# Kernel optimization log

Hardware: AMD Instinct MI355X
Metric: run time of the kernel (lower is better)

Reference implementation:

```python
import jax, jax.numpy as jnp
import numpy as np
from jax import lax

THR = 1.0
SLOPE = 25.0
EPS = 1e-5

@jax.custom_vjp
def spike(u):
    # Heaviside with fast-sigmoid surrogate gradient (slope=25)
    return (u > 0.0).astype(u.dtype)

def _spike_fwd(u):
    return (u > 0.0).astype(u.dtype), u

def _spike_bwd(u, g):
    return (g / (SLOPE * jnp.abs(u) + 1.0) ** 2,)

spike.defvjp(_spike_fwd, _spike_bwd)

def lif_scan(inp, beta):
    # inp: (T, B, H); snntorch Leaky, reset_mechanism='subtract', init mem=0
    def step(mem, cur):
        reset = lax.stop_gradient(spike(mem - THR))
        mem = beta * mem + cur - reset * THR
        spk = spike(mem - THR)
        return mem, (spk, mem)
    mem0 = jnp.zeros(inp.shape[1:], inp.dtype)
    _, (spk, mem) = lax.scan(step, mem0, inp)
    return spk, mem

def bn_per_step(h, g, b):
    # h: (T, B, H); training-mode BatchNorm1d applied per timestep over batch
    m = h.mean(axis=1, keepdims=True)
    v = h.var(axis=1, keepdims=True)
    return (h - m) / jnp.sqrt(v + EPS) * g + b

def setup_inputs() -> dict:
    key = jax.random.key(0)
    ks = jax.random.split(key, 16)
    B, T, C = 128, 128, 32
    H, Ts, HOR, K = 512, 4, 96, 3
    s = 0.02
    return {
        "x": jax.random.normal(ks[0], (B, T, C), jnp.float32),
        "conv_w": jax.random.normal(ks[1], (H * Ts, C, K), jnp.float32) * s,
        "conv_b": jnp.zeros((H * Ts,), jnp.float32),
        "bn1_g": jnp.ones((H * Ts,), jnp.float32),
        "bn1_b": jnp.zeros((H * Ts,), jnp.float32),
        "beta_enc": jnp.full((H,), 0.9, jnp.float32),
        "bn2_g": jnp.ones((H,), jnp.float32),
        "bn2_b": jnp.zeros((H,), jnp.float32),
        "beta2": jnp.full((H,), 0.9, jnp.float32),
        "bn3_g": jnp.ones((H,), jnp.float32),
        "bn3_b": jnp.zeros((H,), jnp.float32),
        "beta3": jnp.full((H,), 0.9, jnp.float32),
        "wq": jax.random.normal(ks[2], (H, H), jnp.float32) * s,
        "bq": jnp.zeros((H,), jnp.float32),
        "wk": jax.random.normal(ks[3], (H, H), jnp.float32) * s,
        "bk": jnp.zeros((H,), jnp.float32),
        "wv": jax.random.normal(ks[4], (H, H), jnp.float32) * s,
        "bv": jnp.zeros((H,), jnp.float32),
        "bna_g": jnp.ones((H,), jnp.float32),
        "bna_b": jnp.zeros((H,), jnp.float32),
        "wh": jax.random.normal(ks[5], (HOR, H), jnp.float32) * s,
        "bh": jnp.zeros((HOR,), jnp.float32),
    }

def reference(x, conv_w, conv_b, bn1_g, bn1_b, beta_enc, bn2_g, bn2_b, beta2,
              bn3_g, bn3_b, beta3, wq, bq, wk, bk, wv, bv, bna_g, bna_b, wh, bh):
    B, T, C = x.shape
    H = beta2.shape[0]
    Ts = conv_w.shape[0] // H
    # Conv spike encoder: Conv1d(C -> H*Ts, k, pad=k//2)
    k = conv_w.shape[2]
    h = lax.conv_general_dilated(x.transpose(0, 2, 1), conv_w, (1,), [(k // 2, k // 2)],
                                 dimension_numbers=("NCH", "OIH", "NCH"))
    h = h + conv_b[None, :, None]  # (B, H*Ts, T)
    # BatchNorm1d (training mode): stats over (B, T) per channel, biased var
    m = h.mean((0, 2), keepdims=True)
    v = h.var((0, 2), keepdims=True)
    h = (h - m) / jnp.sqrt(v + EPS) * bn1_g[None, :, None] + bn1_b[None, :, None]
    # (B, H*Ts, T) -> (T*Ts, B, H)
    h = h.transpose(0, 2, 1).reshape(B, T, Ts, H).reshape(B, T * Ts, H).transpose(1, 0, 2)
    spk_enc, _ = lif_scan(h, jnp.clip(beta_enc, 0.0, 0.99))
    # bn2 -> lif2 -> bn3 -> lif3 (BN applied per step in the torch loop)
    h2 = bn_per_step(spk_enc, bn2_g, bn2_b)
    s2, _ = lif_scan(h2, jnp.clip(beta2, 0.0, 0.99))
    h3 = bn_per_step(s2, bn3_g, bn3_b)
    _, mem3 = lif_scan(h3, jnp.clip(beta3, 0.0, 0.99))  # (Ttot, B, H)
    # Spiking attention over membrane trajectory
    xa = mem3.transpose(1, 0, 2)  # (B, Ttot, H)
    Q = xa @ wq.T + bq
    K = xa @ wk.T + bk
    V = xa @ wv.T + bv
    attn = jax.nn.sigmoid(jnp.einsum("btd,bsd->bts", Q, K) * (H ** -0.5))
    feat = jnp.einsum("bts,bsd->btd", attn, V).mean(axis=1)  # (B, H)
    mf = feat.mean(0, keepdims=True)
    vf = feat.var(0, keepdims=True)
    feat = (feat - mf) / jnp.sqrt(vf + EPS) * bna_g + bna_b
    return feat @ wh.T + bh  # (B, horizon)
```

## Files before the change

### kernel.cpp

```cpp
#include <hip/hip_runtime.h>
#include <math.h>

#define EPSF 1e-5f

static constexpr int Bn   = 128;
static constexpr int Tn   = 128;
static constexpr int Cn   = 32;
static constexpr int On   = 2048;
static constexpr int Hn   = 512;
static constexpr int TTn  = 512;
static constexpr int HORn = 96;
static constexpr int BH   = Bn * Hn;
static constexpr float THRf = 1.0f;

__device__ __forceinline__ float bf2f(unsigned short u) {
    union { unsigned int i; float f; } v; v.i = ((unsigned int)u) << 16; return v.f;
}
__device__ __forceinline__ unsigned short f2bf(float f) {
    union { float f; unsigned int i; } v; v.f = f;
    unsigned int r = v.i + 0x7fff + ((v.i >> 16) & 1);
    return (unsigned short)(r >> 16);
}

using bfrag  = __attribute__((ext_vector_type(8))) short;
using f32x4v = __attribute__((ext_vector_type(4))) float;
using f32x16 = __attribute__((ext_vector_type(16))) float;
using us8v   = __attribute__((ext_vector_type(8))) unsigned short;

#define GLD16(gp, lp) __builtin_amdgcn_global_load_lds( \
    (const __attribute__((address_space(1))) void*)(gp), \
    (__attribute__((address_space(3))) void*)(lp), 16, 0, 0)

__global__ __launch_bounds__(256) void im2col_k(const float* __restrict__ x,
    unsigned short* __restrict__ Ph, unsigned short* __restrict__ Pl)
{
    int idx = blockIdx.x * 256 + threadIdx.x;
    int row = idx / 96, kc = idx - row * 96;
    int k = kc >> 5, c = kc & 31;
    int t = row & 127, b = row >> 7;
    int tg = t + k - 1;
    float v = (tg >= 0 && tg < Tn) ? x[((size_t)b * Tn + tg) * Cn + c] : 0.f;
    unsigned short hi = f2bf(v);
    Ph[idx] = hi;
    Pl[idx] = f2bf(v - bf2f(hi));
}

__global__ __launch_bounds__(256) void wprep_k(const float* __restrict__ wconv,
    unsigned short* __restrict__ Wh, unsigned short* __restrict__ Wl)
{
    int idx = blockIdx.x * 256 + threadIdx.x;
    int o = idx / 96, kc = idx - o * 96;
    int k = kc >> 5, c = kc & 31;
    float v = wconv[(size_t)o * 96 + c * 3 + k];
    unsigned short hi = f2bf(v);
    Wh[idx] = hi;
    Wl[idx] = f2bf(v - bf2f(hi));
}

__global__ __launch_bounds__(256) void conv_mfma_k(
    const unsigned short* __restrict__ Ph, const unsigned short* __restrict__ Pl,
    const unsigned short* __restrict__ Wh, const unsigned short* __restrict__ Wl,
    float* __restrict__ raw, float* __restrict__ sums)
{
    const int b  = blockIdx.x;
    const int n0 = blockIdx.y * 128;
    const int tid = threadIdx.x;
    const int lane = tid & 63;
    const int quad = lane >> 4, lr = lane & 15;
    const int wid = tid >> 6, wm = wid & 1, wn = wid >> 1;

    f32x4v acc[4][4] = {};
#pragma unroll
    for (int ks = 0; ks < 3; ks++) {
        const int col = ks * 32 + quad * 8;
        bfrag ah[4], al[4], bh[4], bl[4];
#pragma unroll
        for (int mi = 0; mi < 4; mi++) {
            size_t roff = ((size_t)b * 128 + wm * 64 + mi * 16 + lr) * 96 + col;
            ah[mi] = *(const bfrag*)(Ph + roff);
            al[mi] = *(const bfrag*)(Pl + roff);
        }
#pragma unroll
        for (int ni = 0; ni < 4; ni++) {
            size_t roff = (size_t)(n0 + wn * 64 + ni * 16 + lr) * 96 + col;
            bh[ni] = *(const bfrag*)(Wh + roff);
            bl[ni] = *(const bfrag*)(Wl + roff);
        }
#pragma unroll
        for (int mi = 0; mi < 4; mi++)
#pragma unroll
            for (int ni = 0; ni < 4; ni++) {
                acc[mi][ni] = __builtin_amdgcn_mfma_f32_16x16x32_bf16(
                    ah[mi], bh[ni], acc[mi][ni], 0, 0, 0);
                acc[mi][ni] = __builtin_amdgcn_mfma_f32_16x16x32_bf16(
                    ah[mi], bl[ni], acc[mi][ni], 0, 0, 0);
                acc[mi][ni] = __builtin_amdgcn_mfma_f32_16x16x32_bf16(
                    al[mi], bh[ni], acc[mi][ni], 0, 0, 0);
            }
    }
#pragma unroll
    for (int ni = 0; ni < 4; ni++) {
        int o = n0 + wn * 64 + ni * 16 + lr;
        int ts = o >> 9, hh = o & 511;
        float s = 0.f, ss = 0.f;
#pragma unroll
        for (int mi = 0; mi < 4; mi++)
#pragma unroll
            for (int r = 0; r < 4; r++) {
                int t = wm * 64 + mi * 16 + quad * 4 + r;
                float v = acc[mi][ni][r];
                raw[((size_t)(t * 4 + ts) * Bn + b) * Hn + hh] = v;
                s += v; ss += v * v;
            }
        s  += __shfl_xor(s, 16);  s  += __shfl_xor(s, 32);
        ss += __shfl_xor(ss, 16); ss += __shfl_xor(ss, 32);
        if (quad == 0) {
            atomicAdd(&sums[o], s);
            atomicAdd(&sums[On + o], ss);
        }
    }
}

__global__ void bn1_final_k(const float* __restrict__ sums,
                            const float* __restrict__ g, const float* __restrict__ bb,
                            float* __restrict__ scale, float* __restrict__ shift)
{
    int o = blockIdx.x * 256 + threadIdx.x;
    float m = sums[o] * (1.f / 16384.f);
    float v = sums[On + o] * (1.f / 16384.f) - m * m;
    float sc = g[o] / sqrtf(v + EPSF);
    scale[o] = sc;
    shift[o] = bb[o] - m * sc;
}

__global__ __launch_bounds__(256) void lif1_k(const float* __restrict__ raw,
    const float* __restrict__ scale, const float* __restrict__ shift,
    const float* __restrict__ beta_in, unsigned char* __restrict__ spk)
{
    const int thr = blockIdx.x * 256 + threadIdx.x;
    const int hh = thr & 511;
    const float beta = fminf(fmaxf(beta_in[hh], 0.f), 0.99f);
    float sc[4], sh[4];
#pragma unroll
    for (int ts = 0; ts < 4; ts++) { sc[ts] = scale[ts * Hn + hh]; sh[ts] = shift[ts * Hn + hh]; }
    float mem = 0.f;
    for (int tt = 0; tt < TTn; tt += 8) {
        float cu[8];
#pragma unroll
        for (int u = 0; u < 8; u++) cu[u] = raw[(size_t)(tt + u) * BH + thr];
#pragma unroll
        for (int u = 0; u < 8; u++) {
            float cur = cu[u] * sc[u & 3] + sh[u & 3];
            float reset = mem > THRf ? 1.f : 0.f;
            mem = beta * mem + cur - reset;
            spk[(size_t)(tt + u) * BH + thr] = mem > THRf ? (unsigned char)1 : (unsigned char)0;
        }
    }
}

__global__ __launch_bounds__(256) void bnstep_k(const unsigned char* __restrict__ spk,
    const float* __restrict__ g, const float* __restrict__ bb,
    float* __restrict__ av, float* __restrict__ zv)
{
    const int tt = blockIdx.x;
    const int h0 = threadIdx.x * 2;
    int c0 = 0, c1 = 0;
    const unsigned char* base = spk + (size_t)tt * BH + h0;
#pragma unroll 8
    for (int b = 0; b < Bn; b++) {
        unsigned short v = *(const unsigned short*)(base + (size_t)b * Hn);
        c0 += (v & 0xff); c1 += (v >> 8);
    }
#pragma unroll
    for (int q = 0; q < 2; q++) {
        int hh = h0 + q;
        float p = (q ? c1 : c0) * (1.f / 128.f);
        float inv = 1.f / sqrtf(p - p * p + EPSF);
        float gi = g[hh] * inv;
        float zz = bb[hh] - p * gi;
        av[(size_t)tt * Hn + hh] = gi + zz;
        zv[(size_t)tt * Hn + hh] = zz;
    }
}

__global__ __launch_bounds__(256) void lif2_k(const unsigned char* __restrict__ sin_,
    const float* __restrict__ av, const float* __restrict__ zv,
    const float* __restrict__ beta_in, unsigned char* __restrict__ sout)
{
    const int thr = blockIdx.x * 256 + threadIdx.x;
    const int hh = thr & 511;
    const float beta = fminf(fmaxf(beta_in[hh], 0.f), 0.99f);
    float mem = 0.f;
    for (int tt = 0; tt < TTn; tt += 8) {
        float aa[8], zz[8]; unsigned char ss[8];
#pragma unroll
        for (int u = 0; u < 8; u++) {
            ss[u] = sin_[(size_t)(tt + u) * BH + thr];
            aa[u] = av[(size_t)(tt + u) * Hn + hh];
            zz[u] = zv[(size_t)(tt + u) * Hn + hh];
        }
#pragma unroll
        for (int u = 0; u < 8; u++) {
            float cur = ss[u] ? aa[u] : zz[u];
            float reset = mem > THRf ? 1.f : 0.f;
            mem = beta * mem + cur - reset;
            sout[(size_t)(tt + u) * BH + thr] = mem > THRf ? (unsigned char)1 : (unsigned char)0;
        }
    }
}

__global__ __launch_bounds__(256) void lif3_k(const unsigned char* __restrict__ sin_,
    const float* __restrict__ av, const float* __restrict__ zv,
    const float* __restrict__ beta_in, unsigned short* __restrict__ mem3b)
{
    const int thr = blockIdx.x * 256 + threadIdx.x;
    const int hh = thr & 511;
    const int b = thr >> 9;
    const float beta = fminf(fmaxf(beta_in[hh], 0.f), 0.99f);
    float mem = 0.f;
    for (int tt = 0; tt < TTn; tt += 8) {
        float aa[8], zz[8]; unsigned char ss[8];
#pragma unroll
        for (int u = 0; u < 8; u++) {
            ss[u] = sin_[(size_t)(tt + u) * BH + thr];
            aa[u] = av[(size_t)(tt + u) * Hn + hh];
            zz[u] = zv[(size_t)(tt + u) * Hn + hh];
        }
#pragma unroll
        for (int u = 0; u < 8; u++) {
            float cur = ss[u] ? aa[u] : zz[u];
            float reset = mem > THRf ? 1.f : 0.f;
            mem = beta * mem + cur - reset;
            mem3b[((size_t)b * TTn + (tt + u)) * Hn + hh] = f2bf(mem);
        }
    }
}

__global__ __launch_bounds__(256) void gemm_atb_k(const float* __restrict__ Aw,
    const float* __restrict__ Bw, float* __restrict__ GTp)
{
    __shared__ float As[8][132];
    __shared__ float Bs[8][132];
    const int m0 = blockIdx.x * 128;
    const int n0 = blockIdx.y * 128;
    const int kz = blockIdx.z;
    const int tid = threadIdx.x;
    const int ir = tid >> 5, cl = (tid & 31) * 4;
    const float* Ap = Aw + (size_t)ir * 512 + m0 + cl;
    const float* Bp = Bw + (size_t)ir * 512 + n0 + cl;
    const int tm = tid & 15, tn = tid >> 4;
    float acc[8][8];
#pragma unroll
    for (int i = 0; i < 8; i++)
#pragma unroll
        for (int j = 0; j < 8; j++) acc[i][j] = 0.f;

    for (int i0 = kz * 64; i0 < kz * 64 + 64; i0 += 8) {
        const float4 avv = *(const float4*)(Ap + (size_t)i0 * 512);
        const float4 bvv = *(const float4*)(Bp + (size_t)i0 * 512);
        __syncthreads();
        *(float4*)&As[ir][cl] = avv;
        *(float4*)&Bs[ir][cl] = bvv;
        __syncthreads();
#pragma unroll
        for (int kk = 0; kk < 8; kk++) {
            float4 a0 = *(const float4*)&As[kk][tm * 8];
            float4 a1 = *(const float4*)&As[kk][tm * 8 + 4];
            float4 b0 = *(const float4*)&Bs[kk][tn * 8];
            float4 b1 = *(const float4*)&Bs[kk][tn * 8 + 4];
            float a_[8] = {a0.x, a0.y, a0.z, a0.w, a1.x, a1.y, a1.z, a1.w};
            float b_[8] = {b0.x, b0.y, b0.z, b0.w, b1.x, b1.y, b1.z, b1.w};
#pragma unroll
            for (int i = 0; i < 8; i++)
#pragma unroll
                for (int j = 0; j < 8; j++) acc[i][j] += a_[i] * b_[j];
        }
    }
    float* outp = GTp + (size_t)kz * Hn * Hn;
#pragma unroll
    for (int i = 0; i < 8; i++) {
        size_t rowoff = (size_t)(m0 + tm * 8 + i) * 512 + n0 + tn * 8;
#pragma unroll
        for (int j = 0; j < 8; j++) outp[rowoff + j] = acc[i][j];
    }
}

__global__ void gtred_k(const float* __restrict__ GTp, unsigned short* __restrict__ GT)
{
    int idx = blockIdx.x * 256 + threadIdx.x;
    float s = 0.f;
#pragma unroll
    for (int z = 0; z < 8; z++) s += GTp[(size_t)z * Hn * Hn + idx];
    GT[idx] = f2bf(s);
}

__global__ __launch_bounds__(256) void bias_prep_k(const float* __restrict__ wq,
    const float* __restrict__ wk, const float* __restrict__ bq,
    const float* __restrict__ bk, float* __restrict__ qb, float* __restrict__ kb)
{
    const int blk = blockIdx.x;
    const bool doq = blk < 8;
    const int d0 = (doq ? blk : blk - 8) * 64;
    const float* W    = doq ? wq : wk;
    const float* bvec = doq ? bk : bq;
    const int dl = threadIdx.x & 63, ig = threadIdx.x >> 6;
    float s = 0.f;
    for (int i = ig * 128; i < ig * 128 + 128; i++)
        s += W[(size_t)i * 512 + d0 + dl] * bvec[i];
    __shared__ float red[4][64];
    red[ig][dl] = s;
    __syncthreads();
    if (ig == 0)
        (doq ? qb : kb)[d0 + dl] = red[0][dl] + red[1][dl] + red[2][dl] + red[3][dl];
}

__global__ void c0_k(const float* __restrict__ bq, const float* __restrict__ bk,
                     float* __restrict__ c0)
{
    __shared__ float red[256];
    float p = 0.f;
    for (int i = threadIdx.x; i < 512; i += 256) p += bq[i] * bk[i];
    red[threadIdx.x] = p;
    __syncthreads();
    for (int s = 128; s > 0; s >>= 1) {
        if (threadIdx.x < s) red[threadIdx.x] += red[threadIdx.x + s];
        __syncthreads();
    }
    if (threadIdx.x == 0) c0[0] = red[0];
}

__global__ __launch_bounds__(256) void ygemm_k(const unsigned short* __restrict__ A,
    const unsigned short* __restrict__ Bsrc, const float* __restrict__ qb,
    const float* __restrict__ kb, const float* __restrict__ c0,
    unsigned short* __restrict__ C, float* __restrict__ rowq,
    float* __restrict__ rowk)
{
    __shared__ unsigned short As[128 * 64];
    __shared__ unsigned short Bs[128 * 64];
    const int m0 = blockIdx.x * 128;
    const int n0 = blockIdx.y * 128;
    const int tid = threadIdx.x;
    const int lane = tid & 63;
    const int l31 = lane & 31, kw = lane >> 5;
    const int wid = tid >> 6;
    const int wm = wid & 1, wn = wid >> 1;

    const int srw = lane >> 3;
    const int scc = (lane & 7) ^ (srw & 7);
    const unsigned short* gA = A    + (size_t)(m0 + wid * 32 + srw) * 512 + scc * 8;
    const unsigned short* gB = Bsrc + (size_t)(n0 + wid * 32 + srw) * 512 + scc * 8;

    const bool dorows = (blockIdx.y == 0) && (wn == 0);
    float rq_acc[2] = {0.f, 0.f};
    float rk_acc[2] = {0.f, 0.f};

    f32x16 acc[2][2] = {};
    for (int k0 = 0; k0 < 512; k0 += 64) {
        __syncthreads();
#pragma unroll
        for (int j = 0; j < 4; j++) {
            GLD16(gA + (size_t)j * 8 * 512 + k0, As + (wid * 32 + j * 8) * 64);
            GLD16(gB + (size_t)j * 8 * 512 + k0, Bs + (wid * 32 + j * 8) * 64);
        }
        __syncthreads();
#pragma unroll
        for (int kk = 0; kk < 4; kk++) {
            const int chunk = kk * 2 + kw;
            bfrag af[2], bf_[2];
#pragma unroll
            for (int mi = 0; mi < 2; mi++) {
                const int row = wm * 64 + mi * 32 + l31;
                af[mi] = *(const bfrag*)&As[row * 64 + (chunk ^ (row & 7)) * 8];
            }
#pragma unroll
            for (int ni = 0; ni < 2; ni++) {
                const int row = wn * 64 + ni * 32 + l31;
                bf_[ni] = *(const bfrag*)&Bs[row * 64 + (chunk ^ (row & 7)) * 8];
            }
#pragma unroll
            for (int mi = 0; mi < 2; mi++)
#pragma unroll
                for (int ni = 0; ni < 2; ni++)
                    acc[mi][ni] = __builtin_amdgcn_mfma_f32_32x32x16_bf16(
                        af[mi], bf_[ni], acc[mi][ni], 0, 0, 0);
            if (dorows) {
                const int koff = k0 + kk * 16 + kw * 8;
                const float4 qv0 = *(const float4*)(qb + koff);
                const float4 qv1 = *(const float4*)(qb + koff + 4);
                const float4 kv0 = *(const float4*)(kb + koff);
                const float4 kv1 = *(const float4*)(kb + koff + 4);
                const float qv[8] = {qv0.x, qv0.y, qv0.z, qv0.w, qv1.x, qv1.y, qv1.z, qv1.w};
                const float kv[8] = {kv0.x, kv0.y, kv0.z, kv0.w, kv1.x, kv1.y, kv1.z, kv1.w};
#pragma unroll
                for (int mi = 0; mi < 2; mi++)
#pragma unroll
                    for (int j = 0; j < 8; j++) {
                        float a = bf2f((unsigned short)af[mi][j]);
                        rq_acc[mi] += a * qv[j];
                        rk_acc[mi] += a * kv[j];
                    }
            }
        }
    }
#pragma unroll
    for (int mi = 0; mi < 2; mi++)
#pragma unroll
        for (int ni = 0; ni < 2; ni++) {
            const int col = n0 + wn * 64 + ni * 32 + l31;
#pragma unroll
            for (int reg = 0; reg < 16; reg++) {
                const int row = m0 + wm * 64 + mi * 32
                              + (reg & 3) + 8 * (reg >> 2) + 4 * kw;
                C[(size_t)row * 512 + col] = f2bf(acc[mi][ni][reg]);
            }
        }
    if (dorows) {
        const float c0v = c0[0];
#pragma unroll
        for (int mi = 0; mi < 2; mi++) {
            float rq = rq_acc[mi], rk = rk_acc[mi];
            rq += __shfl_xor(rq, 32);
            rk += __shfl_xor(rk, 32);
            if (kw == 0) {
                const int row = m0 + wm * 64 + mi * 32 + l31;
                rowq[row] = rq + c0v;
                rowk[row] = rk;
            }
        }
    }
}

__global__ __launch_bounds__(256) void scores_k(const unsigned short* __restrict__ Y,
    const unsigned short* __restrict__ Xm, const float* __restrict__ rowq,
    const float* __restrict__ rowk, float* __restrict__ wacc)
{
    __shared__ unsigned short As[128 * 64];
    __shared__ unsigned short Bs[128 * 64];
    __shared__ float colsum[128];
    __shared__ float rq_s[128], rk_s[128];
    const int b  = blockIdx.z;
    const int m0 = blockIdx.x * 128;
    const int n0 = blockIdx.y * 128;
    const int tid = threadIdx.x;
    const int lane = tid & 63;
    const int l31 = lane & 31, kw = lane >> 5;
    const int wid = tid >> 6;
    const int wm = wid & 1, wn = wid >> 1;

    if (tid < 128) {
        colsum[tid] = 0.f;
        rq_s[tid] = rowq[(size_t)b * TTn + m0 + tid];
        rk_s[tid] = rowk[(size_t)b * TTn + n0 + tid];
    }

    const int srw = lane >> 3;
    const int scc = (lane & 7) ^ (srw & 7);
    const unsigned short* gA = Y  + (size_t)b * TTn * Hn
        + (size_t)(m0 + wid * 32 + srw) * 512 + scc * 8;
    const unsigned short* gB = Xm + (size_t)b * TTn * Hn
        + (size_t)(n0 + wid * 32 + srw) * 512 + scc * 8;

    f32x16 acc[2][2] = {};
    for (int k0 = 0; k0 < 512; k0 += 64) {
        __syncthreads();
#pragma unroll
        for (int j = 0; j < 4; j++) {
            GLD16(gA + (size_t)j * 8 * 512 + k0, As + (wid * 32 + j * 8) * 64);
            GLD16(gB + (size_t)j * 8 * 512 + k0, Bs + (wid * 32 + j * 8) * 64);
        }
        __syncthreads();
#pragma unroll
        for (int kk = 0; kk < 4; kk++) {
            const int chunk = kk * 2 + kw;
            bfrag af[2], bf_[2];
#pragma unroll
            for (int mi = 0; mi < 2; mi++) {
                const int row = wm * 64 + mi * 32 + l31;
                af[mi] = *(const bfrag*)&As[row * 64 + (chunk ^ (row & 7)) * 8];
            }
#pragma unroll
            for (int ni = 0; ni < 2; ni++) {
                const int row = wn * 64 + ni * 32 + l31;
                bf_[ni] = *(const bfrag*)&Bs[row * 64 + (chunk ^ (row & 7)) * 8];
            }
#pragma unroll
            for (int mi = 0; mi < 2; mi++)
#pragma unroll
                for (int ni = 0; ni < 2; ni++)
                    acc[mi][ni] = __builtin_amdgcn_mfma_f32_32x32x16_bf16(
                        af[mi], bf_[ni], acc[mi][ni], 0, 0, 0);
        }
    }
    const float scl = 0.044194173824159216f;
#pragma unroll
    for (int ni = 0; ni < 2; ni++) {
        const int col_l = wn * 64 + ni * 32 + l31;
        const float rkv = rk_s[col_l];
        float s_ln = 0.f;
#pragma unroll
        for (int mi = 0; mi < 2; mi++) {
#pragma unroll
            for (int reg = 0; reg < 16; reg++) {
                const int row_l = wm * 64 + mi * 32
                                + (reg & 3) + 8 * (reg >> 2) + 4 * kw;
                float xv = (acc[mi][ni][reg] + rq_s[row_l] + rkv) * scl;
                s_ln += 1.f / (1.f + __expf(-xv));
            }
        }
        s_ln += __shfl_xor(s_ln, 32);
        if (kw == 0) atomicAdd(&colsum[col_l], s_ln);
    }
    __syncthreads();
    if (tid < 128)
        atomicAdd(&wacc[(size_t)b * TTn + n0 + tid], colsum[tid] * (1.f / 512.f));
}

__global__ __launch_bounds__(256) void wsum_k(const float* __restrict__ wacc,
    const unsigned short* __restrict__ mem3b, float* __restrict__ u,
    float* __restrict__ W1)
{
    const int b = blockIdx.x;
    const int tid = threadIdx.x;
    const int wid = tid >> 6, lane = tid & 63;
    __shared__ float ws_[512];
    __shared__ float part[4][512];
    __shared__ float red[256];
    ws_[tid] = wacc[(size_t)b * TTn + tid];
    ws_[tid + 256] = wacc[(size_t)b * TTn + tid + 256];
    __syncthreads();
    float a[8] = {0.f, 0.f, 0.f, 0.f, 0.f, 0.f, 0.f, 0.f};
    const unsigned short* Xb = mem3b + (size_t)b * TTn * Hn + lane * 8;
    for (int s = wid * 128; s < wid * 128 + 128; s++) {
        const float w = ws_[s];
        const us8v xv = *(const us8v*)(Xb + (size_t)s * Hn);
#pragma unroll
        for (int j = 0; j < 8; j++) a[j] += w * bf2f(xv[j]);
    }
#pragma unroll
    for (int j = 0; j < 8; j++) part[wid][lane * 8 + j] = a[j];
    red[tid] = ws_[tid] + ws_[tid + 256];
    __syncthreads();
    for (int st = 128; st > 0; st >>= 1) {
        if (tid < st) red[tid] += red[tid + st];
        __syncthreads();
    }
    if (tid == 0) W1[b] = red[0];
    if (wid == 0) {
#pragma unroll
        for (int j = 0; j < 8; j++) {
            const int e = lane * 8 + j;
            u[(size_t)b * Hn + e] = part[0][e] + part[1][e] + part[2][e] + part[3][e];
        }
    }
}

__global__ __launch_bounds__(256) void feat2_k(const float* __restrict__ u,
    const float* __restrict__ W1, const float* __restrict__ wv,
    const float* __restrict__ bv, float* __restrict__ feat)
{
    const int b = blockIdx.x;
    const int tid = threadIdx.x;
    __shared__ float us[512];
    us[tid] = u[(size_t)b * Hn + tid];
    us[tid + 256] = u[(size_t)b * Hn + tid + 256];
    __syncthreads();
    const float w1 = W1[b];
#pragma unroll
    for (int q = 0; q < 2; q++) {
        int d = tid + q * 256;
        float acc = bv[d] * w1;
        const float* wr = wv + (size_t)d * 512;
        for (int e = 0; e < 512; e += 4) {
            float4 w4 = *(const float4*)(wr + e);
            acc += us[e] * w4.x + us[e+1] * w4.y + us[e+2] * w4.z + us[e+3] * w4.w;
        }
        feat[(size_t)b * Hn + d] = acc;
    }
}

__global__ void bna_k(const float* __restrict__ feat, const float* __restrict__ g,
                      const float* __restrict__ bb, float* __restrict__ featn)
{
    int d = blockIdx.x * 256 + threadIdx.x;
    float s = 0.f, ss = 0.f;
    for (int b = 0; b < Bn; b++) { float v = feat[(size_t)b * Hn + d]; s += v; ss += v * v; }
    float m = s * (1.f / 128.f);
    float var = ss * (1.f / 128.f) - m * m;
    float sc = g[d] / sqrtf(var + EPSF);
    float sh = bb[d] - m * sc;
    for (int b = 0; b < Bn; b++) featn[(size_t)b * Hn + d] = feat[(size_t)b * Hn + d] * sc + sh;
}

__global__ __launch_bounds__(128) void head_k(const float* __restrict__ featn,
    const float* __restrict__ wh, const float* __restrict__ bh, float* __restrict__ out)
{
    const int b = blockIdx.x;
    __shared__ float f[512];
    const int tid = threadIdx.x;
    for (int i = tid; i < 512; i += 128) f[i] = featn[(size_t)b * Hn + i];
    __syncthreads();
    if (tid < HORn) {
        float accv = bh[tid];
        const float* wr = wh + (size_t)tid * Hn;
        for (int d = 0; d < 512; d++) accv += f[d] * wr[d];
        out[(size_t)b * HORn + tid] = accv;
    }
}

__global__ void dbg_k(float* out, float v) { out[0] = v; }

extern "C" void kernel_launch(void* const* d_in, const int* in_sizes, int n_in,
                              void* d_out, int out_size, void* d_ws, size_t ws_size,
                              hipStream_t stream)
{
    (void)in_sizes; (void)n_in;
    const float* x      = (const float*)d_in[0];
    const float* conv_w = (const float*)d_in[1];
    const float* bn1_g  = (const float*)d_in[3];
    const float* bn1_b  = (const float*)d_in[4];
    const float* beta_e = (const float*)d_in[5];
    const float* bn2_g  = (const float*)d_in[6];
    const float* bn2_b  = (const float*)d_in[7];
    const float* beta2  = (const float*)d_in[8];
    const float* bn3_g  = (const float*)d_in[9];
    const float* bn3_b  = (const float*)d_in[10];
    const float* beta3  = (const float*)d_in[11];
    const float* wq     = (const float*)d_in[12];
    const float* bq     = (const float*)d_in[13];
    const float* wk     = (const float*)d_in[14];
    const float* bk     = (const float*)d_in[15];
    const float* wv     = (const float*)d_in[16];
    const float* bv     = (const float*)d_in[17];
    const float* bna_g  = (const float*)d_in[18];
    const float* bna_b  = (const float*)d_in[19];
    const float* wh     = (const float*)d_in[20];
    const float* bh     = (const float*)d_in[21];
    float* out = (float*)d_out;

    char* ws = (char*)d_ws;
    size_t off = 0;
    auto alloc = [&](size_t bytes) {
        char* p = ws + off;
        off += (bytes + 255) & ~(size_t)255;
        return p;
    };
    float* raw          = (float*)alloc((size_t)TTn * BH * 4);
    unsigned char* spk1 = (unsigned char*)alloc((size_t)TTn * BH);
    unsigned char* s2   = (unsigned char*)alloc((size_t)TTn * BH);
    unsigned short* Ph = (unsigned short*)alloc((size_t)Bn * Tn * 96 * 2);
    unsigned short* Pl = (unsigned short*)alloc((size_t)Bn * Tn * 96 * 2);
    unsigned short* Wh = (unsigned short*)alloc((size_t)On * 96 * 2);
    unsigned short* Wl = (unsigned short*)alloc((size_t)On * 96 * 2);
    float* sums   = (float*)alloc(2 * On * 4);
    float* scale1 = (float*)alloc(On * 4);
    float* shift1 = (float*)alloc(On * 4);
    float* a2     = (float*)alloc((size_t)TTn * Hn * 4);
    float* z2     = (float*)alloc((size_t)TTn * Hn * 4);
    float* a3     = (float*)alloc((size_t)TTn * Hn * 4);
    float* z3     = (float*)alloc((size_t)TTn * Hn * 4);
    float* wacc   = (float*)alloc((size_t)Bn * TTn * 4);
    float* GTp    = (float*)alloc((size_t)8 * Hn * Hn * 4);
    unsigned short* GT = (unsigned short*)alloc((size_t)Hn * Hn * 2);
    float* qb     = (float*)alloc(Hn * 4);
    float* kb     = (float*)alloc(Hn * 4);
    float* c0     = (float*)alloc(256);
    float* rowq   = (float*)alloc((size_t)Bn * TTn * 4);
    float* rowk   = (float*)alloc((size_t)Bn * TTn * 4);
    float* u      = (float*)alloc((size_t)Bn * Hn * 4);
    float* W1     = (float*)alloc(Bn * 4);
    float* feat   = (float*)alloc((size_t)Bn * Hn * 4);
    float* featn  = (float*)alloc((size_t)Bn * Hn * 4);
    unsigned short* mem3b = (unsigned short*)raw;
    unsigned short* Y     = (unsigned short*)spk1;

    if (ws_size < off) {
        hipMemsetAsync(d_out, 0, (size_t)out_size * 4, stream);
        dbg_k<<<1, 1, 0, stream>>>(out, (float)ws_size);
        return;
    }

    hipMemsetAsync(sums, 0, 2 * On * 4, stream);
    hipMemsetAsync(wacc, 0, (size_t)Bn * TTn * 4, stream);

    im2col_k<<<(Bn * Tn * 96) / 256, 256, 0, stream>>>(x, Ph, Pl);
    wprep_k<<<(On * 96) / 256, 256, 0, stream>>>(conv_w, Wh, Wl);
    conv_mfma_k<<<dim3(Bn, On / 128), 256, 0, stream>>>(Ph, Pl, Wh, Wl, raw, sums);
    bn1_final_k<<<On / 256, 256, 0, stream>>>(sums, bn1_g, bn1_b, scale1, shift1);
    lif1_k<<<BH / 256, 256, 0, stream>>>(raw, scale1, shift1, beta_e, spk1);
    bnstep_k<<<TTn, 256, 0, stream>>>(spk1, bn2_g, bn2_b, a2, z2);
    lif2_k<<<BH / 256, 256, 0, stream>>>(spk1, a2, z2, beta2, s2);
    bnstep_k<<<TTn, 256, 0, stream>>>(s2, bn3_g, bn3_b, a3, z3);
    lif3_k<<<BH / 256, 256, 0, stream>>>(s2, a3, z3, beta3, mem3b);
    gemm_atb_k<<<dim3(4, 4, 8), 256, 0, stream>>>(wk, wq, GTp);
    gtred_k<<<(Hn * Hn) / 256, 256, 0, stream>>>(GTp, GT);
    bias_prep_k<<<16, 256, 0, stream>>>(wq, wk, bq, bk, qb, kb);
    c0_k<<<1, 256, 0, stream>>>(bq, bk, c0);
    ygemm_k<<<dim3((Bn * TTn) / 128, Hn / 128), 256, 0, stream>>>(
        mem3b, GT, qb, kb, c0, Y, rowq, rowk);
    scores_k<<<dim3(TTn / 128, TTn / 128, Bn), 256, 0, stream>>>(Y, mem3b, rowq, rowk, wacc);
    wsum_k<<<Bn, 256, 0, stream>>>(wacc, mem3b, u, W1);
    feat2_k<<<Bn, 256, 0, stream>>>(u, W1, wv, bv, feat);
    bna_k<<<Hn / 256, 256, 0, stream>>>(feat, bna_g, bna_b, featn);
    head_k<<<Bn, 128, 0, stream>>>(featn, wh, bh, out);
}
```

Measured before the change: 500.9 us.

## Vectorize bnstep counts, switch scores to 16x16 MFMA, parallelize bna over batch

Measured after the change: 502.1 us. Within noise of the previous version (+0.2%).

```diff
diff --git a/kernel.cpp b/kernel.cpp
--- a/kernel.cpp
+++ b/kernel.cpp
@@ -163,23 +163,39 @@
     float* __restrict__ av, float* __restrict__ zv)
 {
     const int tt = blockIdx.x;
-    const int h0 = threadIdx.x * 2;
-    int c0 = 0, c1 = 0;
-    const unsigned char* base = spk + (size_t)tt * BH + h0;
-#pragma unroll 8
-    for (int b = 0; b < Bn; b++) {
-        unsigned short v = *(const unsigned short*)(base + (size_t)b * Hn);
-        c0 += (v & 0xff); c1 += (v >> 8);
-    }
-#pragma unroll
-    for (int q = 0; q < 2; q++) {
-        int hh = h0 + q;
-        float p = (q ? c1 : c0) * (1.f / 128.f);
-        float inv = 1.f / sqrtf(p - p * p + EPSF);
-        float gi = g[hh] * inv;
-        float zz = bb[hh] - p * gi;
-        av[(size_t)tt * Hn + hh] = gi + zz;
-        zv[(size_t)tt * Hn + hh] = zz;
+    const int tid = threadIdx.x;
+    const int b0 = tid >> 5;
+    const int hseg = (tid & 31) * 16;
+    const unsigned char* base = spk + (size_t)tt * BH;
+    uint4 a4 = make_uint4(0u, 0u, 0u, 0u);
+#pragma unroll
+    for (int i = 0; i < 16; i++) {
+        const int b = b0 + i * 8;
+        const uint4 v = *(const uint4*)(base + (size_t)b * Hn + hseg);
+        a4.x += v.x; a4.y += v.y; a4.z += v.z; a4.w += v.w;
+    }
+    __shared__ uint4 part[8][32];
+    part[b0][tid & 31] = a4;
+    __syncthreads();
+    if (tid < 32) {
+        uint4 s = part[0][tid];
+#pragma unroll
+        for (int i = 1; i < 8; i++) {
+            uint4 p = part[i][tid];
+            s.x += p.x; s.y += p.y; s.z += p.z; s.w += p.w;
+        }
+        unsigned int w[4] = {s.x, s.y, s.z, s.w};
+#pragma unroll
+        for (int q = 0; q < 16; q++) {
+            int cnt = (w[q >> 2] >> ((q & 3) * 8)) & 0xff;
+            int hh = tid * 16 + q;
+            float p = cnt * (1.f / 128.f);
+            float inv = 1.f / sqrtf(p - p * p + EPSF);
+            float gi = g[hh] * inv;
+            float zz = bb[hh] - p * gi;
+            av[(size_t)tt * Hn + hh] = gi + zz;
+            zv[(size_t)tt * Hn + hh] = zz;
+        }
     }
 }
 
@@ -443,7 +459,7 @@
     const int n0 = blockIdx.y * 128;
     const int tid = threadIdx.x;
     const int lane = tid & 63;
-    const int l31 = lane & 31, kw = lane >> 5;
+    const int quad = lane >> 4, lr = lane & 15;
     const int wid = tid >> 6;
     const int wm = wid & 1, wn = wid >> 1;
 
@@ -460,7 +476,7 @@
     const unsigned short* gB = Xm + (size_t)b * TTn * Hn
         + (size_t)(n0 + wid * 32 + srw) * 512 + scc * 8;
 
-    f32x16 acc[2][2] = {};
+    f32x4v acc[4][4] = {};
     for (int k0 = 0; k0 < 512; k0 += 64) {
         __syncthreads();
 #pragma unroll
@@ -470,45 +486,38 @@
         }
         __syncthreads();
 #pragma unroll
-        for (int kk = 0; kk < 4; kk++) {
-            const int chunk = kk * 2 + kw;
-            bfrag af[2], bf_[2];
-#pragma unroll
-            for (int mi = 0; mi < 2; mi++) {
-                const int row = wm * 64 + mi * 32 + l31;
-                af[mi] = *(const bfrag*)&As[row * 64 + (chunk ^ (row & 7)) * 8];
-            }
-#pragma unroll
-            for (int ni = 0; ni < 2; ni++) {
-                const int row = wn * 64 + ni * 32 + l31;
-                bf_[ni] = *(const bfrag*)&Bs[row * 64 + (chunk ^ (row & 7)) * 8];
-            }
-#pragma unroll
-            for (int mi = 0; mi < 2; mi++)
-#pragma unroll
-                for (int ni = 0; ni < 2; ni++)
-                    acc[mi][ni] = __builtin_amdgcn_mfma_f32_32x32x16_bf16(
+        for (int kk = 0; kk < 2; kk++) {
+            const int slot = (kk * 4 + quad) ^ (lr & 7);
+            bfrag af[4], bf_[4];
+#pragma unroll
+            for (int mi = 0; mi < 4; mi++)
+                af[mi] = *(const bfrag*)&As[(wm * 64 + mi * 16 + lr) * 64 + slot * 8];
+#pragma unroll
+            for (int ni = 0; ni < 4; ni++)
+                bf_[ni] = *(const bfrag*)&Bs[(wn * 64 + ni * 16 + lr) * 64 + slot * 8];
+#pragma unroll
+            for (int mi = 0; mi < 4; mi++)
+#pragma unroll
+                for (int ni = 0; ni < 4; ni++)
+                    acc[mi][ni] = __builtin_amdgcn_mfma_f32_16x16x32_bf16(
                         af[mi], bf_[ni], acc[mi][ni], 0, 0, 0);
         }
     }
     const float scl = 0.044194173824159216f;
 #pragma unroll
-    for (int ni = 0; ni < 2; ni++) {
-        const int col_l = wn * 64 + ni * 32 + l31;
-        const float rkv = rk_s[col_l];
+    for (int ni = 0; ni < 4; ni++) {
         float s_ln = 0.f;
-#pragma unroll
-        for (int mi = 0; mi < 2; mi++) {
-#pragma unroll
-            for (int reg = 0; reg < 16; reg++) {
-                const int row_l = wm * 64 + mi * 32
-                                + (reg & 3) + 8 * (reg >> 2) + 4 * kw;
-                float xv = (acc[mi][ni][reg] + rq_s[row_l] + rkv) * scl;
+        float rkv = rk_s[wn * 64 + ni * 16 + lr];
+#pragma unroll
+        for (int mi = 0; mi < 4; mi++) {
+#pragma unroll
+            for (int r = 0; r < 4; r++) {
+                float rqv = rq_s[wm * 64 + mi * 16 + quad * 4 + r];
+                float xv = (acc[mi][ni][r] + rqv + rkv) * scl;
                 s_ln += 1.f / (1.f + __expf(-xv));
             }
         }
-        s_ln += __shfl_xor(s_ln, 32);
-        if (kw == 0) atomicAdd(&colsum[col_l], s_ln);
+        atomicAdd(&colsum[wn * 64 + ni * 16 + lr], s_ln);
     }
     __syncthreads();
     if (tid < 128)
@@ -578,17 +587,34 @@
     }
 }
 
-__global__ void bna_k(const float* __restrict__ feat, const float* __restrict__ g,
-                      const float* __restrict__ bb, float* __restrict__ featn)
-{
-    int d = blockIdx.x * 256 + threadIdx.x;
+__global__ __launch_bounds__(256) void bna_k(const float* __restrict__ feat,
+    const float* __restrict__ g, const float* __restrict__ bb,
+    float* __restrict__ featn)
+{
+    const int d0 = blockIdx.x * 64;
+    const int dl = threadIdx.x & 63, bg = threadIdx.x >> 6;
     float s = 0.f, ss = 0.f;
-    for (int b = 0; b < Bn; b++) { float v = feat[(size_t)b * Hn + d]; s += v; ss += v * v; }
-    float m = s * (1.f / 128.f);
-    float var = ss * (1.f / 128.f) - m * m;
-    float sc = g[d] / sqrtf(var + EPSF);
-    float sh = bb[d] - m * sc;
-    for (int b = 0; b < Bn; b++) featn[(size_t)b * Hn + d] = feat[(size_t)b * Hn + d] * sc + sh;
+    for (int b = bg * 32; b < bg * 32 + 32; b++) {
+        float v = feat[(size_t)b * Hn + d0 + dl];
+        s += v; ss += v * v;
+    }
+    __shared__ float ls[4][64], lss[4][64];
+    __shared__ float sc_s[64], sh_s[64];
+    ls[bg][dl] = s; lss[bg][dl] = ss;
+    __syncthreads();
+    if (threadIdx.x < 64) {
+        float st  = ls[0][dl] + ls[1][dl] + ls[2][dl] + ls[3][dl];
+        float sst = lss[0][dl] + lss[1][dl] + lss[2][dl] + lss[3][dl];
+        float m = st * (1.f / 128.f);
+        float var = sst * (1.f / 128.f) - m * m;
+        float sc = g[d0 + dl] / sqrtf(var + EPSF);
+        sc_s[dl] = sc;
+        sh_s[dl] = bb[d0 + dl] - m * sc;
+    }
+    __syncthreads();
+    for (int b = bg * 32; b < bg * 32 + 32; b++)
+        featn[(size_t)b * Hn + d0 + dl] =
+            feat[(size_t)b * Hn + d0 + dl] * sc_s[dl] + sh_s[dl];
 }
 
 __global__ __launch_bounds__(128) void head_k(const float* __restrict__ featn,
@@ -700,6 +726,6 @@
     scores_k<<<dim3(TTn / 128, TTn / 128, Bn), 256, 0, stream>>>(Y, mem3b, rowq, rowk, wacc);
     wsum_k<<<Bn, 256, 0, stream>>>(wacc, mem3b, u, W1);
     feat2_k<<<Bn, 256, 0, stream>>>(u, W1, wv, bv, feat);
-    bna_k<<<Hn / 256, 256, 0, stream>>>(feat, bna_g, bna_b, featn);
+    bna_k<<<Hn / 64, 256, 0, stream>>>(feat, bna_g, bna_b, featn);
     head_k<<<Bn, 128, 0, stream>>>(featn, wh, bh, out);
 }
```
